# Optimization experiments

Measured on AMD Instinct MI355X. Metric: run time of the kernel, lower is better.

## Reference

```python
import jax, jax.numpy as jnp
import numpy as np

B, S, D, H, W = 4, 4096, 1024, 16, 128
HD = D // H


def setup_inputs() -> dict:
    key = jax.random.key(0)
    ks = jax.random.split(key, 12)
    s = 1.0 / np.sqrt(D)
    return {
        "query": jax.random.normal(ks[0], (B, S, D), jnp.float32),
        "key": jax.random.normal(ks[1], (B, S, D), jnp.float32),
        "value": jax.random.normal(ks[2], (B, S, D), jnp.float32),
        "Wq": jax.random.normal(ks[3], (D, D), jnp.float32) * s,
        "bq": jnp.zeros((D,), jnp.float32),
        "Wk": jax.random.normal(ks[4], (D, D), jnp.float32) * s,
        "bk": jnp.zeros((D,), jnp.float32),
        "Wv": jax.random.normal(ks[5], (D, D), jnp.float32) * s,
        "bv": jnp.zeros((D,), jnp.float32),
        "Wo": jax.random.normal(ks[6], (D, D), jnp.float32) * s,
        "bo": jnp.zeros((D,), jnp.float32),
        "global_indices": jnp.arange(32, dtype=jnp.int32),
    }


def _mha(q, k, v, Wq, bq, Wk, bk, Wv, bv, Wo, bo):
    # q,k,v: [..., S, D]; full multi-head attention over the last-but-one axis.
    def split(x):
        return x.reshape(x.shape[:-1] + (H, HD))
    qh = split(q @ Wq.T + bq)
    kh = split(k @ Wk.T + bk)
    vh = split(v @ Wv.T + bv)
    scale = 1.0 / np.sqrt(HD)
    scores = jnp.einsum('...qhd,...khd->...hqk', qh, kh) * scale
    attn = jax.nn.softmax(scores, axis=-1)
    out = jnp.einsum('...hqk,...khd->...qhd', attn, vh)
    out = out.reshape(q.shape)
    return out @ Wo.T + bo


def reference(query, key, value, Wq, bq, Wk, bk, Wv, bv, Wo, bo, global_indices):
    nW = S // W
    # non-overlapping windowed attention: [B, nW, W, D]
    qw = query.reshape(B, nW, W, D)
    kw = key.reshape(B, nW, W, D)
    vw = value.reshape(B, nW, W, D)
    local = _mha(qw, kw, vw, Wq, bq, Wk, bk, Wv, bv, Wo, bo).reshape(B, S, D)
    # global-token pass: attention among global tokens only
    gq = query[:, global_indices]
    gk = key[:, global_indices]
    gv = value[:, global_indices]
    gout = _mha(gq, gk, gv, Wq, bq, Wk, bk, Wv, bv, Wo, bo)
    return local.at[:, global_indices].set(gout)
```

## Files before the change

kernel.cpp:

```cpp
#include <hip/hip_runtime.h>

#define DB 4
#define SS 4096
#define DD 1024
#define HH 16
#define HD 64
#define WW 128
#define NW 32
#define NG 32

typedef __bf16 bf16_t;
typedef bf16_t bf16x4 __attribute__((ext_vector_type(4)));
typedef bf16_t bf16x8 __attribute__((ext_vector_type(8)));
typedef float f32x4 __attribute__((ext_vector_type(4)));

typedef const __attribute__((address_space(1))) void* gptr_t;
typedef __attribute__((address_space(3))) void* lptr_t;

static __device__ __forceinline__ f32x4 mfma16(bf16x8 a, bf16x8 b, f32x4 c) {
    return __builtin_amdgcn_mfma_f32_16x16x32_bf16(a, b, c, 0, 0, 0);
}

__global__ void detect_dtype(const unsigned short* __restrict__ q, int* __restrict__ flag) {
    int lane = threadIdx.x;
    unsigned short u = q[2 * lane];
    bf16_t b;
    __builtin_memcpy(&b, &u, 2);
    float v = fabsf((float)b);
    bool ok = (v > 1e-5f) && (v < 1e5f);
    unsigned long long m = __ballot(ok);
    if (lane == 0) *flag = (__popcll(m) >= 32) ? 1 : 0;
}

__global__ void cvt_x(const void* __restrict__ src, bf16_t* __restrict__ dst,
                      const int* __restrict__ flag) {
    int i = blockIdx.x * blockDim.x + threadIdx.x;
    int e = i * 4;
    if (*flag) {
        *(ushort4*)(dst + e) = ((const ushort4*)src)[i];
    } else {
        float4 f = ((const float4*)src)[i];
        bf16x4 o = { (bf16_t)f.x, (bf16_t)f.y, (bf16_t)f.z, (bf16_t)f.w };
        *(bf16x4*)(dst + e) = o;
    }
}

__global__ void cvt_w(const void* __restrict__ src, bf16_t* __restrict__ wp,
                      const int* __restrict__ flag) {
    int i = blockIdx.x * blockDim.x + threadIdx.x;
    int e = i * 4;
    if (*flag) {
        *(ushort4*)(wp + e) = ((const ushort4*)src)[i];
    } else {
        float4 f = ((const float4*)src)[i];
        bf16x4 h = { (bf16_t)f.x, (bf16_t)f.y, (bf16_t)f.z, (bf16_t)f.w };
        *(bf16x4*)(wp + e) = h;
    }
}

__global__ void cvt_bias(const void* b0, const void* b1, const void* b2, const void* b3,
                         float* __restrict__ dst, const int* __restrict__ flag) {
    int i = blockIdx.x * blockDim.x + threadIdx.x;
    const void* s = (i >> 10) == 0 ? b0 : (i >> 10) == 1 ? b1 : (i >> 10) == 2 ? b2 : b3;
    int j = i & 1023;
    dst[i] = (*flag) ? (float)((const bf16_t*)s)[j] : ((const float*)s)[j];
}

#define GFENCE() asm volatile("" ::: "memory")
#define MIDBAR() do { GFENCE(); __builtin_amdgcn_s_barrier(); GFENCE(); } while (0)
#define ENDBAR(N) do { asm volatile("s_waitcnt vmcnt(" #N ")" ::: "memory"); \
                       __builtin_amdgcn_s_barrier(); GFENCE(); } while (0)

#define QUAD_MFMA(MS, NS, BB)                                                          \
    do {                                                                               \
        __builtin_amdgcn_s_setprio(1);                                                 \
        _Pragma("unroll")                                                              \
        for (int t_ = 0; t_ < 4; ++t_) {                                               \
            _Pragma("unroll")                                                          \
            for (int u_ = 0; u_ < 2; ++u_) {                                           \
                acc[(MS)*4 + t_][(NS)*2 + u_] =                                        \
                    mfma16(a[t_][0], BB[u_][0], acc[(MS)*4 + t_][(NS)*2 + u_]);        \
                acc[(MS)*4 + t_][(NS)*2 + u_] =                                        \
                    mfma16(a[t_][1], BB[u_][1], acc[(MS)*4 + t_][(NS)*2 + u_]);        \
            }                                                                          \
        }                                                                              \
        __builtin_amdgcn_s_setprio(0);                                                 \
    } while (0)

__global__ __launch_bounds__(512, 2) void gemm8(const bf16_t* __restrict__ X,
                                                const bf16_t* __restrict__ Wp,
                                                const float* __restrict__ bias,
                                                void* __restrict__ Yout,
                                                const int* __restrict__ flag,
                                                int final_out) {
    __shared__ alignas(16) bf16_t sA[2][16384];
    __shared__ alignas(16) bf16_t sB[2][16384];

    const int tid  = threadIdx.x;
    const int lane = tid & 63;
    const int wv   = tid >> 6;
    const int c    = lane & 15;
    const int quad = lane >> 4;
    const int wi   = wv >> 2;
    const int wj   = wv & 3;

    const int f32out = final_out ? (*flag == 0) : 0;

    int wg = blockIdx.x;
    wg = (wg & 7) * 32 + (wg >> 3);
    const int mbase = (wg >> 2) * 256;
    const int nbase = (wg & 3) * 256;

    const int d0   = tid * 16;
    const int srow = d0 >> 7;
    const int scol = (d0 & 127) ^ ((srow & 7) << 4);
    const char* srcA = (const char*)X + (size_t)(mbase + srow) * 2048 + scol;
    const char* srcB = (const char*)Wp +
        (size_t)(nbase + ((srow >> 5) << 6) + (srow & 31)) * 2048 + scol;
    char* const ldsA = (char*)&sA[0][0] + wv * 1024;
    char* const ldsB = (char*)&sB[0][0] + wv * 1024;

    f32x4 acc[8][4] = {};
    const int colX = (quad * 16) ^ ((c & 7) << 4);

    auto stageA = [&](int P, int chunk, int ktb) {
        const char* s0 = srcA + ktb + chunk * 131072;
        char* l0 = ldsA + P * 32768 + chunk * 16384;
        __builtin_amdgcn_global_load_lds((gptr_t)s0,            (lptr_t)l0,          16, 0, 0);
        __builtin_amdgcn_global_load_lds((gptr_t)(s0 + 262144), (lptr_t)(l0 + 8192), 16, 0, 0);
    };
    auto stageB = [&](int P, int chunk, int ktb) {
        const char* s0 = srcB + ktb + chunk * 65536;
        char* l0 = ldsB + P * 32768 + chunk * 16384;
        __builtin_amdgcn_global_load_lds((gptr_t)s0,            (lptr_t)l0,          16, 0, 0);
        __builtin_amdgcn_global_load_lds((gptr_t)(s0 + 262144), (lptr_t)(l0 + 8192), 16, 0, 0);
    };

    bf16x8 a[4][2], b0[2][2], b1[2][2];

    auto ldA = [&](int P, int ms) {
        const char* base = (const char*)&sA[0][0] + P * 32768 +
                           (size_t)(ms * 128 + wi * 64 + c) * 128;
        #pragma unroll
        for (int t = 0; t < 4; ++t) {
            a[t][0] = *(const bf16x8*)(base + t * 2048 + colX);
            a[t][1] = *(const bf16x8*)(base + t * 2048 + (colX ^ 64));
        }
    };
    auto ldB0 = [&](int P) {
        const char* base = (const char*)&sB[0][0] + P * 32768 +
                           (size_t)(wj * 32 + c) * 128;
        #pragma unroll
        for (int u = 0; u < 2; ++u) {
            b0[u][0] = *(const bf16x8*)(base + u * 2048 + colX);
            b0[u][1] = *(const bf16x8*)(base + u * 2048 + (colX ^ 64));
        }
    };
    auto ldB1 = [&](int P) {
        const char* base = (const char*)&sB[0][0] + P * 32768 + 16384 +
                           (size_t)(wj * 32 + c) * 128;
        #pragma unroll
        for (int u = 0; u < 2; ++u) {
            b1[u][0] = *(const bf16x8*)(base + u * 2048 + colX);
            b1[u][1] = *(const bf16x8*)(base + u * 2048 + (colX ^ 64));
        }
    };

    stageA(0, 0, 0); stageB(0, 0, 0);
    stageA(0, 1, 0); stageB(0, 1, 0);
    ENDBAR(4);

    int kk = 128;
    for (int t = 0; t < 15; ++t) {
        const int P = t & 1, Q = P ^ 1;
        ldA(P, 0); ldB0(P);
        stageA(Q, 0, kk);
        MIDBAR();
        QUAD_MFMA(0, 0, b0);
        ENDBAR(2);
        ldB1(P);
        stageB(Q, 0, kk);
        MIDBAR();
        QUAD_MFMA(0, 1, b1);
        MIDBAR();
        ldA(P, 1);
        stageA(Q, 1, kk);
        MIDBAR();
        QUAD_MFMA(1, 1, b1);
        MIDBAR();
        stageB(Q, 1, kk);
        MIDBAR();
        QUAD_MFMA(1, 0, b0);
        ENDBAR(4);
        kk += 128;
    }
    ENDBAR(0);
    ldA(1, 0); ldB0(1); ldB1(1);
    QUAD_MFMA(0, 0, b0);
    QUAD_MFMA(0, 1, b1);
    ldA(1, 1);
    QUAD_MFMA(1, 1, b1);
    QUAD_MFMA(1, 0, b0);

    #pragma unroll
    for (int n = 0; n < 4; ++n) {
        const int col = nbase + wj * 64 + (n >> 1) * 32 + (n & 1) * 16 + c;
        const float bv = bias[col];
        #pragma unroll
        for (int m = 0; m < 8; ++m) {
            const int row = mbase + wi * 128 + (m >> 2) * 64 + (m & 3) * 16 + quad * 4;
            #pragma unroll
            for (int r = 0; r < 4; ++r) {
                const float yv = acc[m][n][r] + bv;
                const size_t idx = (size_t)(row + r) * DD + col;
                if (f32out) ((float*)Yout)[idx] = yv;
                else        ((bf16_t*)Yout)[idx] = (bf16_t)yv;
            }
        }
    }
}

__global__ __launch_bounds__(256) void attn_local(const bf16_t* __restrict__ Q,
                                                  const bf16_t* __restrict__ K,
                                                  const bf16_t* __restrict__ V,
                                                  bf16_t* __restrict__ ctx) {
    const int wx = blockIdx.x, h = blockIdx.y, b = blockIdx.z;
    const int tid  = threadIdx.x;
    const int lane = tid & 63;
    const int wv   = tid >> 6;
    const int c    = lane & 15;
    const int quad = lane >> 4;

    __shared__ alignas(16) bf16_t pbuf[128][136];
    __shared__ alignas(16) bf16_t vtb[64][136];

    const size_t base = ((size_t)b * SS + (size_t)wx * WW) * DD + (size_t)h * HD;

    for (int e = tid; e < WW * HD; e += 256) {
        int j = e >> 6, d = e & 63;
        vtb[d][j] = V[base + (size_t)j * DD + d];
    }

    const float scale = 0.125f;

    #pragma unroll
    for (int ii = 0; ii < 2; ++ii) {
        const int it = wv * 2 + ii;
        f32x4 s[8] = {};
        #pragma unroll
        for (int kt = 0; kt < 2; ++kt) {
            bf16x8 a = *(const bf16x8*)(Q + base + (size_t)(it * 16 + c) * DD + kt * 32 + quad * 8);
            #pragma unroll
            for (int jt = 0; jt < 8; ++jt) {
                bf16x8 bb = *(const bf16x8*)(K + base + (size_t)(jt * 16 + c) * DD + kt * 32 + quad * 8);
                s[jt] = mfma16(a, bb, s[jt]);
            }
        }
        #pragma unroll
        for (int jt = 0; jt < 8; ++jt) s[jt] *= scale;

        #pragma unroll
        for (int r = 0; r < 4; ++r) {
            float m = -1e30f;
            #pragma unroll
            for (int jt = 0; jt < 8; ++jt) m = fmaxf(m, s[jt][r]);
            #pragma unroll
            for (int off = 1; off < 16; off <<= 1) m = fmaxf(m, __shfl_xor(m, off));
            float p[8], sum = 0.f;
            #pragma unroll
            for (int jt = 0; jt < 8; ++jt) { p[jt] = __expf(s[jt][r] - m); sum += p[jt]; }
            #pragma unroll
            for (int off = 1; off < 16; off <<= 1) sum += __shfl_xor(sum, off);
            float inv = 1.0f / sum;
            int row = it * 16 + quad * 4 + r;
            #pragma unroll
            for (int jt = 0; jt < 8; ++jt) pbuf[row][jt * 16 + c] = (bf16_t)(p[jt] * inv);
        }
    }

    __syncthreads();

    #pragma unroll
    for (int ii = 0; ii < 2; ++ii) {
        const int it = wv * 2 + ii;
        f32x4 o[4] = {};
        #pragma unroll
        for (int kt = 0; kt < 4; ++kt) {
            bf16x8 a = *(const bf16x8*)&pbuf[it * 16 + c][kt * 32 + quad * 8];
            #pragma unroll
            for (int dt = 0; dt < 4; ++dt) {
                bf16x8 bb = *(const bf16x8*)&vtb[dt * 16 + c][kt * 32 + quad * 8];
                o[dt] = mfma16(a, bb, o[dt]);
            }
        }
        #pragma unroll
        for (int dt = 0; dt < 4; ++dt)
            #pragma unroll
            for (int r = 0; r < 4; ++r)
                ctx[base + (size_t)(it * 16 + quad * 4 + r) * DD + dt * 16 + c] = (bf16_t)(o[dt][r]);
    }
}

__global__ __launch_bounds__(256) void attn_global(const bf16_t* __restrict__ Q,
                                                   const bf16_t* __restrict__ K,
                                                   const bf16_t* __restrict__ V,
                                                   const int* __restrict__ gidx,
                                                   bf16_t* __restrict__ ctx) {
    const int h = blockIdx.x, b = blockIdx.y;
    const int tid = threadIdx.x;

    __shared__ float qs[NG][HD], ks[NG][HD], vs[NG][HD];
    __shared__ float sc[NG][NG + 1];
    __shared__ int gi[NG];

    if (tid < NG) gi[tid] = gidx[tid];
    __syncthreads();

    for (int e = tid; e < NG * HD; e += 256) {
        int i = e >> 6, d = e & 63;
        size_t off = ((size_t)b * SS + gi[i]) * DD + (size_t)h * HD + d;
        qs[i][d] = (float)Q[off];
        ks[i][d] = (float)K[off];
        vs[i][d] = (float)V[off];
    }
    __syncthreads();

    for (int e = tid; e < NG * NG; e += 256) {
        int i = e >> 5, j = e & 31;
        float s = 0.f;
        #pragma unroll 8
        for (int d = 0; d < HD; ++d) s += qs[i][d] * ks[j][d];
        sc[i][j] = s * 0.125f;
    }
    __syncthreads();

    if (tid < NG) {
        float m = -1e30f;
        for (int j = 0; j < NG; ++j) m = fmaxf(m, sc[tid][j]);
        float sum = 0.f;
        for (int j = 0; j < NG; ++j) { float p = __expf(sc[tid][j] - m); sc[tid][j] = p; sum += p; }
        float inv = 1.f / sum;
        for (int j = 0; j < NG; ++j) sc[tid][j] *= inv;
    }
    __syncthreads();

    for (int e = tid; e < NG * HD; e += 256) {
        int i = e >> 6, d = e & 63;
        float o = 0.f;
        #pragma unroll 8
        for (int j = 0; j < NG; ++j) o += sc[i][j] * vs[j][d];
        ctx[((size_t)b * SS + gi[i]) * DD + (size_t)h * HD + d] = (bf16_t)o;
    }
}

extern "C" void kernel_launch(void* const* d_in, const int* in_sizes, int n_in,
                              void* d_out, int out_size, void* d_ws, size_t ws_size,
                              hipStream_t stream) {
    const void* query = d_in[0];
    const void* key_  = d_in[1];
    const void* value = d_in[2];
    const void* Wq = d_in[3];  const void* bq = d_in[4];
    const void* Wk = d_in[5];  const void* bk = d_in[6];
    const void* Wv = d_in[7];  const void* bv = d_in[8];
    const void* Wo = d_in[9];  const void* bo = d_in[10];
    const int* gidx = (const int*)d_in[11];

    const size_t nTok = (size_t)DB * SS * DD;

    int*    flag    = (int*)d_ws;
    float*  biasbuf = (float*)((char*)d_ws + 256);
    bf16_t* Xh      = (bf16_t*)((char*)d_ws + 32768);
    bf16_t* Qp      = Xh + nTok;
    bf16_t* Kp      = Qp + nTok;
    bf16_t* ctx     = Xh;
    bf16_t* Wop     = Kp;

    bf16_t* Wlo = (bf16_t*)d_out;
    bf16_t* Vp  = (bf16_t*)d_out + nTok;

    detect_dtype<<<1, 64, 0, stream>>>((const unsigned short*)query, flag);
    cvt_bias<<<16, 256, 0, stream>>>(bq, bk, bv, bo, biasbuf, flag);

    cvt_w<<<1024, 256, 0, stream>>>(Wq, Wlo, flag);
    cvt_x<<<16384, 256, 0, stream>>>(query, Xh, flag);
    gemm8<<<256, 512, 0, stream>>>(Xh, Wlo, biasbuf + 0, Qp, flag, 0);

    cvt_w<<<1024, 256, 0, stream>>>(Wk, Wlo, flag);
    cvt_x<<<16384, 256, 0, stream>>>(key_, Xh, flag);
    gemm8<<<256, 512, 0, stream>>>(Xh, Wlo, biasbuf + 1024, Kp, flag, 0);

    cvt_w<<<1024, 256, 0, stream>>>(Wv, Wlo, flag);
    cvt_x<<<16384, 256, 0, stream>>>(value, Xh, flag);
    gemm8<<<256, 512, 0, stream>>>(Xh, Wlo, biasbuf + 2048, Vp, flag, 0);

    attn_local<<<dim3(NW, HH, DB), 256, 0, stream>>>(Qp, Kp, Vp, ctx);
    attn_global<<<dim3(HH, DB), 256, 0, stream>>>(Qp, Kp, Vp, gidx, ctx);

    cvt_w<<<1024, 256, 0, stream>>>(Wo, Wop, flag);
    gemm8<<<256, 512, 0, stream>>>(ctx, Wop, biasbuf + 3072, d_out, flag, 1);
}
```

Measured before the change: 505.2 us.

## Preload Q/K fragments, swizzle P buffer, vectorize V transpose, merge setup kernels

The local attention kernel now loads each wave's K and Q MFMA fragments into registers once, instead of re-reading K from global memory for every query tile. It also builds the transposed V tile with 8-wide vector stores to LDS and uses an XOR-swizzled, unpadded P buffer to avoid bank conflicts, with launch bounds asking for 3 blocks per CU. Separately, the global-attention softmax runs as wave-parallel shuffles instead of 32 serial threads, and dtype detection is fused with bias conversion to save one launch. The register preloads raise register pressure, which may hurt occupancy.

```diff
diff --git a/kernel.cpp b/kernel.cpp
--- a/kernel.cpp
+++ b/kernel.cpp
@@ -21,15 +21,27 @@
     return __builtin_amdgcn_mfma_f32_16x16x32_bf16(a, b, c, 0, 0, 0);
 }
 
-__global__ void detect_dtype(const unsigned short* __restrict__ q, int* __restrict__ flag) {
-    int lane = threadIdx.x;
-    unsigned short u = q[2 * lane];
-    bf16_t b;
-    __builtin_memcpy(&b, &u, 2);
-    float v = fabsf((float)b);
-    bool ok = (v > 1e-5f) && (v < 1e5f);
-    unsigned long long m = __ballot(ok);
-    if (lane == 0) *flag = (__popcll(m) >= 32) ? 1 : 0;
+__global__ void detect_and_bias(const unsigned short* __restrict__ q, int* __restrict__ flag,
+                                const void* b0, const void* b1, const void* b2, const void* b3,
+                                float* __restrict__ dst) {
+    __shared__ int sflag;
+    int tid = threadIdx.x;
+    if (tid < 64) {
+        unsigned short u = q[2 * tid];
+        bf16_t b;
+        __builtin_memcpy(&b, &u, 2);
+        float v = fabsf((float)b);
+        bool ok = (v > 1e-5f) && (v < 1e5f);
+        unsigned long long m = __ballot(ok);
+        if (tid == 0) { int f = (__popcll(m) >= 32) ? 1 : 0; *flag = f; sflag = f; }
+    }
+    __syncthreads();
+    const int f = sflag;
+    for (int i = tid; i < 4096; i += 256) {
+        const void* s = (i >> 10) == 0 ? b0 : (i >> 10) == 1 ? b1 : (i >> 10) == 2 ? b2 : b3;
+        int j = i & 1023;
+        dst[i] = f ? (float)((const bf16_t*)s)[j] : ((const float*)s)[j];
+    }
 }
 
 __global__ void cvt_x(const void* __restrict__ src, bf16_t* __restrict__ dst,
@@ -56,14 +68,6 @@
         bf16x4 h = { (bf16_t)f.x, (bf16_t)f.y, (bf16_t)f.z, (bf16_t)f.w };
         *(bf16x4*)(wp + e) = h;
     }
-}
-
-__global__ void cvt_bias(const void* b0, const void* b1, const void* b2, const void* b3,
-                         float* __restrict__ dst, const int* __restrict__ flag) {
-    int i = blockIdx.x * blockDim.x + threadIdx.x;
-    const void* s = (i >> 10) == 0 ? b0 : (i >> 10) == 1 ? b1 : (i >> 10) == 2 ? b2 : b3;
-    int j = i & 1023;
-    dst[i] = (*flag) ? (float)((const bf16_t*)s)[j] : ((const float*)s)[j];
 }
 
 #define GFENCE() asm volatile("" ::: "memory")
@@ -220,10 +224,10 @@
     }
 }
 
-__global__ __launch_bounds__(256) void attn_local(const bf16_t* __restrict__ Q,
-                                                  const bf16_t* __restrict__ K,
-                                                  const bf16_t* __restrict__ V,
-                                                  bf16_t* __restrict__ ctx) {
+__global__ __launch_bounds__(256, 3) void attn_local(const bf16_t* __restrict__ Q,
+                                                     const bf16_t* __restrict__ K,
+                                                     const bf16_t* __restrict__ V,
+                                                     bf16_t* __restrict__ ctx) {
     const int wx = blockIdx.x, h = blockIdx.y, b = blockIdx.z;
     const int tid  = threadIdx.x;
     const int lane = tid & 63;
@@ -231,14 +235,35 @@
     const int c    = lane & 15;
     const int quad = lane >> 4;
 
-    __shared__ alignas(16) bf16_t pbuf[128][136];
+    __shared__ alignas(16) bf16_t pbuf[128][128];
     __shared__ alignas(16) bf16_t vtb[64][136];
 
     const size_t base = ((size_t)b * SS + (size_t)wx * WW) * DD + (size_t)h * HD;
 
-    for (int e = tid; e < WW * HD; e += 256) {
-        int j = e >> 6, d = e & 63;
-        vtb[d][j] = V[base + (size_t)j * DD + d];
+    bf16x8 kf[8][2], qf[2][2];
+    #pragma unroll
+    for (int jt = 0; jt < 8; ++jt)
+        #pragma unroll
+        for (int kt = 0; kt < 2; ++kt)
+            kf[jt][kt] = *(const bf16x8*)(K + base + (size_t)(jt * 16 + c) * DD + kt * 32 + quad * 8);
+    #pragma unroll
+    for (int ii = 0; ii < 2; ++ii)
+        #pragma unroll
+        for (int kt = 0; kt < 2; ++kt)
+            qf[ii][kt] = *(const bf16x8*)(Q + base + (size_t)((wv * 2 + ii) * 16 + c) * DD + kt * 32 + quad * 8);
+
+    {
+        const int vd  = tid & 63;
+        const int vj0 = (tid >> 6) * 8;
+        #pragma unroll
+        for (int pass = 0; pass < 4; ++pass) {
+            const int j0 = vj0 + pass * 32;
+            bf16_t tmp[8];
+            #pragma unroll
+            for (int u = 0; u < 8; ++u)
+                tmp[u] = V[base + (size_t)(j0 + u) * DD + vd];
+            *(bf16x8*)&vtb[vd][j0] = *(const bf16x8*)tmp;
+        }
     }
 
     const float scale = 0.125f;
@@ -248,14 +273,10 @@
         const int it = wv * 2 + ii;
         f32x4 s[8] = {};
         #pragma unroll
-        for (int kt = 0; kt < 2; ++kt) {
-            bf16x8 a = *(const bf16x8*)(Q + base + (size_t)(it * 16 + c) * DD + kt * 32 + quad * 8);
-            #pragma unroll
-            for (int jt = 0; jt < 8; ++jt) {
-                bf16x8 bb = *(const bf16x8*)(K + base + (size_t)(jt * 16 + c) * DD + kt * 32 + quad * 8);
-                s[jt] = mfma16(a, bb, s[jt]);
-            }
-        }
+        for (int kt = 0; kt < 2; ++kt)
+            #pragma unroll
+            for (int jt = 0; jt < 8; ++jt)
+                s[jt] = mfma16(qf[ii][kt], kf[jt][kt], s[jt]);
         #pragma unroll
         for (int jt = 0; jt < 8; ++jt) s[jt] *= scale;
 
@@ -272,9 +293,12 @@
             #pragma unroll
             for (int off = 1; off < 16; off <<= 1) sum += __shfl_xor(sum, off);
             float inv = 1.0f / sum;
-            int row = it * 16 + quad * 4 + r;
-            #pragma unroll
-            for (int jt = 0; jt < 8; ++jt) pbuf[row][jt * 16 + c] = (bf16_t)(p[jt] * inv);
+            const int row = it * 16 + quad * 4 + r;
+            char* pb = (char*)pbuf;
+            #pragma unroll
+            for (int jt = 0; jt < 8; ++jt)
+                *(bf16_t*)(pb + ((row * 256 + (jt * 16 + c) * 2) ^ ((row & 7) << 4))) =
+                    (bf16_t)(p[jt] * inv);
         }
     }
 
@@ -283,10 +307,13 @@
     #pragma unroll
     for (int ii = 0; ii < 2; ++ii) {
         const int it = wv * 2 + ii;
+        const int prow = it * 16 + c;
+        const char* pb = (const char*)pbuf;
         f32x4 o[4] = {};
         #pragma unroll
         for (int kt = 0; kt < 4; ++kt) {
-            bf16x8 a = *(const bf16x8*)&pbuf[it * 16 + c][kt * 32 + quad * 8];
+            bf16x8 a = *(const bf16x8*)(pb +
+                ((prow * 256 + (kt * 32 + quad * 8) * 2) ^ ((prow & 7) << 4)));
             #pragma unroll
             for (int dt = 0; dt < 4; ++dt) {
                 bf16x8 bb = *(const bf16x8*)&vtb[dt * 16 + c][kt * 32 + quad * 8];
@@ -334,13 +361,17 @@
     }
     __syncthreads();
 
-    if (tid < NG) {
-        float m = -1e30f;
-        for (int j = 0; j < NG; ++j) m = fmaxf(m, sc[tid][j]);
-        float sum = 0.f;
-        for (int j = 0; j < NG; ++j) { float p = __expf(sc[tid][j] - m); sc[tid][j] = p; sum += p; }
-        float inv = 1.f / sum;
-        for (int j = 0; j < NG; ++j) sc[tid][j] *= inv;
+    for (int i = tid >> 5; i < NG; i += 8) {
+        const int j = tid & 31;
+        float v = sc[i][j];
+        float m = v;
+        #pragma unroll
+        for (int off = 1; off < 32; off <<= 1) m = fmaxf(m, __shfl_xor(m, off));
+        float p = __expf(v - m);
+        float s = p;
+        #pragma unroll
+        for (int off = 1; off < 32; off <<= 1) s += __shfl_xor(s, off);
+        sc[i][j] = p / s;
     }
     __syncthreads();
 
@@ -378,8 +409,8 @@
     bf16_t* Wlo = (bf16_t*)d_out;
     bf16_t* Vp  = (bf16_t*)d_out + nTok;
 
-    detect_dtype<<<1, 64, 0, stream>>>((const unsigned short*)query, flag);
-    cvt_bias<<<16, 256, 0, stream>>>(bq, bk, bv, bo, biasbuf, flag);
+    detect_and_bias<<<1, 256, 0, stream>>>((const unsigned short*)query, flag,
+                                           bq, bk, bv, bo, biasbuf);
 
     cvt_w<<<1024, 256, 0, stream>>>(Wq, Wlo, flag);
     cvt_x<<<16384, 256, 0, stream>>>(query, Xh, flag);
```

Result: faster. 494.6 us (-2.1%).
